# Kernel optimization log

Measured on AMD Instinct MI355X. Metric: run time of the kernel, lower is better.

## Reference

```python
import jax, jax.numpy as jnp
import numpy as np

B, BEV = 2, 128
Q = BEV * BEV          # 16384 BEV queries
C, H, L, P = 256, 8, 1, 4
D = C // H             # 32 per-head dim


def setup_inputs() -> dict:
    key = jax.random.key(0)
    ks = jax.random.split(key, 14)
    s = 0.02
    return {
        "query": jax.random.normal(ks[0], (B, Q, C), jnp.float32),
        "value": jax.random.normal(ks[1], (B, Q, C), jnp.float32),
        "identity": jax.random.normal(ks[2], (B, Q, C), jnp.float32),
        "query_pos": jax.random.normal(ks[3], (B, Q, C), jnp.float32),
        "reference_points": jax.random.uniform(ks[4], (B, Q, L, 2), jnp.float32),
        "spatial_shapes": jnp.array([[BEV, BEV]], jnp.int32),
        "level_start_index": jnp.array([0], jnp.int32),
        "Wv": jax.random.normal(ks[5], (C, C), jnp.float32) * s,
        "bv": jnp.zeros((C,), jnp.float32),
        "Woff": jax.random.normal(ks[6], (C, H * L * P * 2), jnp.float32) * s,
        "boff": jax.random.normal(ks[7], (H * L * P * 2,), jnp.float32) * s,
        "Ww": jax.random.normal(ks[8], (C, H * L * P), jnp.float32) * s,
        "bw": jnp.zeros((H * L * P,), jnp.float32),
        "Wo": jax.random.normal(ks[9], (C, C), jnp.float32) * s,
        "bo": jnp.zeros((C,), jnp.float32),
    }


def _deform_attn(q, v, reference_points, shapes_np, Wv, bv, Woff, boff, Ww, bw, Wo, bo):
    b, nq, _ = q.shape
    v = v @ Wv + bv                                             # value_proj
    off = (q @ Woff + boff).reshape(b, nq, H, L, P, 2)          # sampling offsets
    attn = jax.nn.softmax((q @ Ww + bw).reshape(b, nq, H, L * P), axis=-1)
    attn = attn.reshape(b, nq, H, L, P)
    # offset normalizer is (W, H) per level
    norm = jnp.asarray(shapes_np[:, ::-1], jnp.float32)         # [L, 2]
    loc = reference_points[:, :, None, :, None, :] + off / norm[None, None, None, :, None, :]

    out = jnp.zeros((b, H, nq, D), jnp.float32)
    start = 0
    for l in range(L):
        Hl, Wl = int(shapes_np[l, 0]), int(shapes_np[l, 1])
        N = Hl * Wl
        vl = v[:, start:start + N].reshape(b, N, H, D).transpose(0, 2, 1, 3)  # [b,H,N,D]
        start += N
        ll = loc[:, :, :, l]                                    # [b,nq,H,P,2] in [0,1]
        # grid_sample(align_corners=False): pixel coord = loc*size - 0.5
        x = ll[..., 0] * Wl - 0.5
        y = ll[..., 1] * Hl - 0.5
        x0 = jnp.floor(x); y0 = jnp.floor(y)
        dx = x - x0; dy = y - y0
        x0i = x0.astype(jnp.int32); y0i = y0.astype(jnp.int32)

        def gather(ix, iy):
            valid = (ix >= 0) & (ix < Wl) & (iy >= 0) & (iy < Hl)  # zero padding
            idx = jnp.clip(iy, 0, Hl - 1) * Wl + jnp.clip(ix, 0, Wl - 1)
            idx = idx.transpose(0, 2, 1, 3).reshape(b, H, nq * P)
            g = jnp.take_along_axis(vl, idx[..., None], axis=2)   # [b,H,nq*P,D]
            return g * valid.transpose(0, 2, 1, 3).reshape(b, H, nq * P, 1)

        def cw(w):  # corner weight -> [b,H,nq*P,1]
            return w.transpose(0, 2, 1, 3).reshape(b, H, nq * P, 1)

        samp = (gather(x0i, y0i) * cw((1 - dx) * (1 - dy))
                + gather(x0i + 1, y0i) * cw(dx * (1 - dy))
                + gather(x0i, y0i + 1) * cw((1 - dx) * dy)
                + gather(x0i + 1, y0i + 1) * cw(dx * dy))
        samp = samp.reshape(b, H, nq, P, D)
        aw = attn[:, :, :, l].transpose(0, 2, 1, 3)             # [b,H,nq,P]
        out = out + jnp.einsum('bhqpd,bhqp->bhqd', samp, aw)

    out = out.transpose(0, 2, 1, 3).reshape(b, nq, C)
    return out @ Wo + bo                                        # output_proj


def reference(query, value, identity, query_pos, reference_points, spatial_shapes,
              level_start_index, Wv, bv, Woff, boff, Ww, bw, Wo, bo):
    shapes_np = np.asarray(spatial_shapes)                      # static level shapes
    q = query + query_pos
    out = _deform_attn(q, value, reference_points, shapes_np,
                       Wv, bv, Woff, boff, Ww, bw, Wo, bo)
    return out + identity
```

## Files before the change

### kernel.cpp

```cpp
#include <hip/hip_runtime.h>
#include <hip/hip_bf16.h>
#include <stdint.h>

#define Q_TOT 32768
#define CC 256
#define GRID_W 128
#define GRID_H 128

typedef __attribute__((ext_vector_type(8))) short short8;
typedef __attribute__((ext_vector_type(4))) float floatx4;

__device__ __forceinline__ ushort f2bf(float f) {
    union { float f; uint32_t u; } v; v.f = f;
    uint32_t r = (v.u + 0x7fffu + ((v.u >> 16) & 1u)) >> 16;
    return (ushort)r;
}
__device__ __forceinline__ void bf2x2(uint32_t u, float& lo, float& hi) {
    union { uint32_t u; float f; } a, b;
    a.u = u << 16; b.u = u & 0xffff0000u;
    lo = a.f; hi = b.f;
}
__device__ __forceinline__ void async_load16(const void* g, void* l) {
    __builtin_amdgcn_global_load_lds(
        reinterpret_cast<const __attribute__((address_space(1))) uint32_t*>(
            reinterpret_cast<uintptr_t>(g)),
        reinterpret_cast<__attribute__((address_space(3))) uint32_t*>(
            reinterpret_cast<uintptr_t>(l)),
        16, 0, 0);
}

__global__ __launch_bounds__(256)
void prep_weights(const float* __restrict__ Wv, const float* __restrict__ Wo,
                  const float* __restrict__ Woff, const float* __restrict__ Ww,
                  const float* __restrict__ boff, const float* __restrict__ bw,
                  ushort* __restrict__ WvT, ushort* __restrict__ WoT,
                  ushort* __restrict__ WowT, float* __restrict__ bias_ow)
{
    int idx = blockIdx.x * blockDim.x + threadIdx.x;
    if (idx < 65536) {
        int n = idx >> 8, k = idx & 255;
        WvT[idx] = f2bf(Wv[k * 256 + n]);
    } else if (idx < 131072) {
        int t = idx - 65536; int n = t >> 8, k = t & 255;
        WoT[t] = f2bf(Wo[k * 256 + n]);
    } else if (idx < 155648) {
        int t = idx - 131072; int n = t >> 8, k = t & 255;
        float v = (n < 64) ? Woff[k * 64 + n] : Ww[k * 32 + (n - 64)];
        WowT[t] = f2bf(v);
    } else if (idx < 155744) {
        int t = idx - 155648;
        bias_ow[t] = (t < 64) ? boff[t] : bw[t - 64];
    }
}

template <int BM, int BN, int WAVE_M, int WAVE_N, bool OUT_BF16, int CONV>
__global__ __launch_bounds__(256)
void gemm_bf16(const void* __restrict__ Av, const float* __restrict__ A2,
               const ushort* __restrict__ Bt,
               const float* __restrict__ bias, const float* __restrict__ res,
               void* __restrict__ Cout, int M, int N, int K)
{
    constexpr int TM = BM / WAVE_M / 16;
    constexpr int TN = BN / WAVE_N / 16;
    __shared__ __align__(16) ushort As[2][BM * 32];
    __shared__ __align__(16) ushort Bs[2][BN * 32];

    const int tid = threadIdx.x;
    const int lane = tid & 63;
    const int wave = tid >> 6;
    const int wm = wave / WAVE_N;
    const int wn = wave % WAVE_N;
    const int quad = lane >> 4;
    const int m16 = lane & 15;
    const int lrow = lane >> 2;
    const int lkk = (lane & 3) * 8;

    const int nwg = gridDim.x * gridDim.y;
    const int hw = blockIdx.y * gridDim.x + blockIdx.x;
    const int t = (hw & 7) * (nwg >> 3) + (hw >> 3);
    const int bx = t % gridDim.x;
    const int by = t / gridDim.x;

    const int row0 = by * BM;
    const int col0 = bx * BN;

    floatx4 acc[TM][TN] = {};

    auto stage = [&](int buf, int k0) {
        #pragma unroll
        for (int i = wave; i < BM / 16; i += 4) {
            const int r = row0 + i * 16 + lrow;
            if constexpr (CONV == 0) {
                const ushort* src = (const ushort*)Av + (size_t)r * K + (k0 + lkk);
                async_load16(src, &As[buf][i * 16 * 32]);
            } else {
                const float* src = (const float*)Av + (size_t)r * K + (k0 + lkk);
                float4 a0 = ((const float4*)src)[0];
                float4 a1 = ((const float4*)src)[1];
                if constexpr (CONV == 2) {
                    const float* s2 = A2 + (size_t)r * K + (k0 + lkk);
                    float4 b0 = ((const float4*)s2)[0];
                    float4 b1 = ((const float4*)s2)[1];
                    a0.x += b0.x; a0.y += b0.y; a0.z += b0.z; a0.w += b0.w;
                    a1.x += b1.x; a1.y += b1.y; a1.z += b1.z; a1.w += b1.w;
                }
                uint4 o;
                o.x = ((uint32_t)f2bf(a0.y) << 16) | f2bf(a0.x);
                o.y = ((uint32_t)f2bf(a0.w) << 16) | f2bf(a0.z);
                o.z = ((uint32_t)f2bf(a1.y) << 16) | f2bf(a1.x);
                o.w = ((uint32_t)f2bf(a1.w) << 16) | f2bf(a1.z);
                *(uint4*)&As[buf][i * 16 * 32 + lrow * 32 + lkk] = o;
            }
        }
        #pragma unroll
        for (int i = wave; i < BN / 16; i += 4) {
            const ushort* src = Bt + (size_t)(col0 + i * 16 + lrow) * K + (k0 + lkk);
            async_load16(src, &Bs[buf][i * 16 * 32]);
        }
    };

    stage(0, 0);
    __syncthreads();

    int cur = 0;
    for (int k0 = 0; k0 < K; k0 += 32) {
        if (k0 + 32 < K) stage(cur ^ 1, k0 + 32);

        short8 af[TM], bfr[TN];
        #pragma unroll
        for (int i = 0; i < TM; ++i)
            af[i] = *(const short8*)&As[cur][(wm * TM * 16 + i * 16 + m16) * 32 + quad * 8];
        #pragma unroll
        for (int j = 0; j < TN; ++j)
            bfr[j] = *(const short8*)&Bs[cur][(wn * TN * 16 + j * 16 + m16) * 32 + quad * 8];
        #pragma unroll
        for (int i = 0; i < TM; ++i)
            #pragma unroll
            for (int j = 0; j < TN; ++j)
                acc[i][j] = __builtin_amdgcn_mfma_f32_16x16x32_bf16(
                    af[i], bfr[j], acc[i][j], 0, 0, 0);

        __syncthreads();
        cur ^= 1;
    }

    #pragma unroll
    for (int i = 0; i < TM; ++i) {
        #pragma unroll
        for (int j = 0; j < TN; ++j) {
            const int gcol = col0 + wn * TN * 16 + j * 16 + m16;
            const float bb = bias[gcol];
            #pragma unroll
            for (int r = 0; r < 4; ++r) {
                const int grow = row0 + wm * TM * 16 + i * 16 + quad * 4 + r;
                float v = acc[i][j][r] + bb;
                if (res) v += res[(size_t)grow * N + gcol];
                if constexpr (OUT_BF16)
                    ((ushort*)Cout)[(size_t)grow * N + gcol] = f2bf(v);
                else
                    ((float*)Cout)[(size_t)grow * N + gcol] = v;
            }
        }
    }
}

#define QB 8
__global__ __launch_bounds__(256)
void sample_kernel(const ushort* __restrict__ v2,
                   const ushort* __restrict__ ow,
                   const float* __restrict__ ref,
                   ushort* __restrict__ out)
{
    const int tid = threadIdx.x;
    const int ql = tid >> 5;
    const int h  = (tid >> 2) & 7;
    const int dg = tid & 3;
    const int q = blockIdx.x * QB + ql;
    const int b = q >> 14;

    const ushort* op = ow + (size_t)q * 96 + h * 8;
    const uint4 oraw = *(const uint4*)op;
    float offs[8];
    bf2x2(oraw.x, offs[0], offs[1]);
    bf2x2(oraw.y, offs[2], offs[3]);
    bf2x2(oraw.z, offs[4], offs[5]);
    bf2x2(oraw.w, offs[6], offs[7]);

    const uint2 wraw = *(const uint2*)(ow + (size_t)q * 96 + 64 + h * 4);
    float w0, w1, w2, w3;
    bf2x2(wraw.x, w0, w1);
    bf2x2(wraw.y, w2, w3);
    float m = fmaxf(fmaxf(w0, w1), fmaxf(w2, w3));
    float e0 = __expf(w0 - m), e1 = __expf(w1 - m), e2 = __expf(w2 - m), e3 = __expf(w3 - m);
    float inv = 1.f / (e0 + e1 + e2 + e3);
    float aw[4] = {e0 * inv, e1 * inv, e2 * inv, e3 * inv};

    const float rx = ref[(size_t)q * 2 + 0];
    const float ry = ref[(size_t)q * 2 + 1];
    const ushort* vb = v2 + (size_t)b * 16384 * 256 + h * 32 + dg * 8;

    float acc[8] = {};
    #pragma unroll
    for (int p = 0; p < 4; ++p) {
        float x = rx * (float)GRID_W + offs[p * 2 + 0] - 0.5f;
        float y = ry * (float)GRID_H + offs[p * 2 + 1] - 0.5f;
        float x0f = floorf(x), y0f = floorf(y);
        float dx = x - x0f, dy = y - y0f;
        int x0 = (int)x0f, y0 = (int)y0f;
        int x1 = x0 + 1, y1 = y0 + 1;
        float vx0 = (x0 >= 0 && x0 < GRID_W) ? 1.f : 0.f;
        float vx1 = (x1 >= 0 && x1 < GRID_W) ? 1.f : 0.f;
        float vy0 = (y0 >= 0 && y0 < GRID_H) ? 1.f : 0.f;
        float vy1 = (y1 >= 0 && y1 < GRID_H) ? 1.f : 0.f;
        int xc0 = min(max(x0, 0), GRID_W - 1), xc1 = min(max(x1, 0), GRID_W - 1);
        int yc0 = min(max(y0, 0), GRID_H - 1), yc1 = min(max(y1, 0), GRID_H - 1);
        float cw00 = aw[p] * (1.f - dx) * (1.f - dy) * vx0 * vy0;
        float cw10 = aw[p] * dx * (1.f - dy) * vx1 * vy0;
        float cw01 = aw[p] * (1.f - dx) * dy * vx0 * vy1;
        float cw11 = aw[p] * dx * dy * vx1 * vy1;
        const int base0 = yc0 * GRID_W, base1 = yc1 * GRID_W;
        const uint4 r00 = *(const uint4*)(vb + (size_t)(base0 + xc0) * 256);
        const uint4 r10 = *(const uint4*)(vb + (size_t)(base0 + xc1) * 256);
        const uint4 r01 = *(const uint4*)(vb + (size_t)(base1 + xc0) * 256);
        const uint4 r11 = *(const uint4*)(vb + (size_t)(base1 + xc1) * 256);
        float lo, hi;
        bf2x2(r00.x, lo, hi); acc[0] += cw00 * lo; acc[1] += cw00 * hi;
        bf2x2(r00.y, lo, hi); acc[2] += cw00 * lo; acc[3] += cw00 * hi;
        bf2x2(r00.z, lo, hi); acc[4] += cw00 * lo; acc[5] += cw00 * hi;
        bf2x2(r00.w, lo, hi); acc[6] += cw00 * lo; acc[7] += cw00 * hi;
        bf2x2(r10.x, lo, hi); acc[0] += cw10 * lo; acc[1] += cw10 * hi;
        bf2x2(r10.y, lo, hi); acc[2] += cw10 * lo; acc[3] += cw10 * hi;
        bf2x2(r10.z, lo, hi); acc[4] += cw10 * lo; acc[5] += cw10 * hi;
        bf2x2(r10.w, lo, hi); acc[6] += cw10 * lo; acc[7] += cw10 * hi;
        bf2x2(r01.x, lo, hi); acc[0] += cw01 * lo; acc[1] += cw01 * hi;
        bf2x2(r01.y, lo, hi); acc[2] += cw01 * lo; acc[3] += cw01 * hi;
        bf2x2(r01.z, lo, hi); acc[4] += cw01 * lo; acc[5] += cw01 * hi;
        bf2x2(r01.w, lo, hi); acc[6] += cw01 * lo; acc[7] += cw01 * hi;
        bf2x2(r11.x, lo, hi); acc[0] += cw11 * lo; acc[1] += cw11 * hi;
        bf2x2(r11.y, lo, hi); acc[2] += cw11 * lo; acc[3] += cw11 * hi;
        bf2x2(r11.z, lo, hi); acc[4] += cw11 * lo; acc[5] += cw11 * hi;
        bf2x2(r11.w, lo, hi); acc[6] += cw11 * lo; acc[7] += cw11 * hi;
    }

    uint4 o;
    o.x = ((uint32_t)f2bf(acc[1]) << 16) | f2bf(acc[0]);
    o.y = ((uint32_t)f2bf(acc[3]) << 16) | f2bf(acc[2]);
    o.z = ((uint32_t)f2bf(acc[5]) << 16) | f2bf(acc[4]);
    o.w = ((uint32_t)f2bf(acc[7]) << 16) | f2bf(acc[6]);
    *(uint4*)(out + (size_t)q * 256 + h * 32 + dg * 8) = o;
}

extern "C" void kernel_launch(void* const* d_in, const int* in_sizes, int n_in,
                              void* d_out, int out_size, void* d_ws, size_t ws_size,
                              hipStream_t stream) {
    const float* query     = (const float*)d_in[0];
    const float* value     = (const float*)d_in[1];
    const float* identity  = (const float*)d_in[2];
    const float* query_pos = (const float*)d_in[3];
    const float* refpts    = (const float*)d_in[4];
    const float* Wv   = (const float*)d_in[7];
    const float* bv   = (const float*)d_in[8];
    const float* Woff = (const float*)d_in[9];
    const float* boff = (const float*)d_in[10];
    const float* Ww   = (const float*)d_in[11];
    const float* bw   = (const float*)d_in[12];
    const float* Wo   = (const float*)d_in[13];
    const float* bo   = (const float*)d_in[14];
    float* out = (float*)d_out;

    char* ws = (char*)d_ws;
    ushort* v2_bf    = (ushort*)(ws);
    ushort* ow_bf    = (ushort*)(ws + 16777216);
    ushort* samp_bf  = (ushort*)(ws + 23068672);
    ushort* WvT      = (ushort*)(ws + 39845888);
    ushort* WoT      = (ushort*)(ws + 39976960);
    ushort* WowT     = (ushort*)(ws + 40108032);
    float*  bias_ow  = (float*)(ws + 40157184);

    prep_weights<<<609, 256, 0, stream>>>(Wv, Wo, Woff, Ww, boff, bw,
                                          WvT, WoT, WowT, bias_ow);
    gemm_bf16<128, 64, 2, 2, true, 1><<<dim3(4, 256), 256, 0, stream>>>(
        value, nullptr, WvT, bv, nullptr, v2_bf, Q_TOT, 256, 256);
    gemm_bf16<32, 96, 2, 2, true, 2><<<dim3(1, 1024), 256, 0, stream>>>(
        query, query_pos, WowT, bias_ow, nullptr, ow_bf, Q_TOT, 96, 256);
    sample_kernel<<<dim3(Q_TOT / QB), 256, 0, stream>>>(v2_bf, ow_bf, refpts, samp_bf);
    gemm_bf16<128, 64, 2, 2, false, 0><<<dim3(4, 256), 256, 0, stream>>>(
        samp_bf, nullptr, WoT, bo, identity, out, Q_TOT, 256, 256);
}
```

Baseline: 253.9 us.

## Fuse offset/weight projection, bilinear sampling and output projection into one kernel

After: 230.5 us. -9.2%, faster.

```diff
diff --git a/kernel.cpp b/kernel.cpp
--- a/kernel.cpp
+++ b/kernel.cpp
@@ -32,9 +32,8 @@
 __global__ __launch_bounds__(256)
 void prep_weights(const float* __restrict__ Wv, const float* __restrict__ Wo,
                   const float* __restrict__ Woff, const float* __restrict__ Ww,
-                  const float* __restrict__ boff, const float* __restrict__ bw,
                   ushort* __restrict__ WvT, ushort* __restrict__ WoT,
-                  ushort* __restrict__ WowT, float* __restrict__ bias_ow)
+                  ushort* __restrict__ WowT)
 {
     int idx = blockIdx.x * blockDim.x + threadIdx.x;
     if (idx < 65536) {
@@ -47,9 +46,6 @@
         int t = idx - 131072; int n = t >> 8, k = t & 255;
         float v = (n < 64) ? Woff[k * 64 + n] : Ww[k * 32 + (n - 64)];
         WowT[t] = f2bf(v);
-    } else if (idx < 155744) {
-        int t = idx - 155648;
-        bias_ow[t] = (t < 64) ? boff[t] : bw[t - 64];
     }
 }
 
@@ -164,90 +160,208 @@
     }
 }
 
-#define QB 8
+#define FBM 64
 __global__ __launch_bounds__(256)
-void sample_kernel(const ushort* __restrict__ v2,
-                   const ushort* __restrict__ ow,
-                   const float* __restrict__ ref,
-                   ushort* __restrict__ out)
+void fused_attn(const float* __restrict__ query, const float* __restrict__ qpos,
+                const ushort* __restrict__ WowT,
+                const float* __restrict__ boff, const float* __restrict__ bw,
+                const ushort* __restrict__ v2,
+                const float* __restrict__ ref,
+                const ushort* __restrict__ WoT,
+                const float* __restrict__ bo, const float* __restrict__ identity,
+                float* __restrict__ out)
 {
+    __shared__ __align__(16) char smem[71680];
+    ushort* As   = (ushort*)smem;
+    ushort* Bsow = (ushort*)(smem + 4096);
+    float*  owl  = (float*)(smem + 10240);
+    ushort* samp = (ushort*)(smem + 36864);
+    ushort* Bwo  = (ushort*)smem;
+
     const int tid = threadIdx.x;
-    const int ql = tid >> 5;
-    const int h  = (tid >> 2) & 7;
-    const int dg = tid & 3;
-    const int q = blockIdx.x * QB + ql;
-    const int b = q >> 14;
-
-    const ushort* op = ow + (size_t)q * 96 + h * 8;
-    const uint4 oraw = *(const uint4*)op;
-    float offs[8];
-    bf2x2(oraw.x, offs[0], offs[1]);
-    bf2x2(oraw.y, offs[2], offs[3]);
-    bf2x2(oraw.z, offs[4], offs[5]);
-    bf2x2(oraw.w, offs[6], offs[7]);
-
-    const uint2 wraw = *(const uint2*)(ow + (size_t)q * 96 + 64 + h * 4);
-    float w0, w1, w2, w3;
-    bf2x2(wraw.x, w0, w1);
-    bf2x2(wraw.y, w2, w3);
-    float m = fmaxf(fmaxf(w0, w1), fmaxf(w2, w3));
-    float e0 = __expf(w0 - m), e1 = __expf(w1 - m), e2 = __expf(w2 - m), e3 = __expf(w3 - m);
-    float inv = 1.f / (e0 + e1 + e2 + e3);
-    float aw[4] = {e0 * inv, e1 * inv, e2 * inv, e3 * inv};
-
-    const float rx = ref[(size_t)q * 2 + 0];
-    const float ry = ref[(size_t)q * 2 + 1];
-    const ushort* vb = v2 + (size_t)b * 16384 * 256 + h * 32 + dg * 8;
-
-    float acc[8] = {};
+    const int lane = tid & 63;
+    const int wave = tid >> 6;
+    const int quad = lane >> 4;
+    const int m16 = lane & 15;
+    const int lrow = lane >> 2;
+    const int lkk = (lane & 3) * 8;
+    const int wm = wave >> 1;
+    const int wn = wave & 1;
+
+    const int q0 = blockIdx.x * FBM;
+
+    floatx4 aow[2][3] = {};
+    for (int k0 = 0; k0 < 256; k0 += 32) {
+        {
+            const int r = wave * 16 + lrow;
+            const float* s1 = query + (size_t)(q0 + r) * 256 + (k0 + lkk);
+            const float* s2 = qpos  + (size_t)(q0 + r) * 256 + (k0 + lkk);
+            float4 a0 = ((const float4*)s1)[0];
+            float4 a1 = ((const float4*)s1)[1];
+            float4 b0 = ((const float4*)s2)[0];
+            float4 b1 = ((const float4*)s2)[1];
+            a0.x += b0.x; a0.y += b0.y; a0.z += b0.z; a0.w += b0.w;
+            a1.x += b1.x; a1.y += b1.y; a1.z += b1.z; a1.w += b1.w;
+            uint4 o;
+            o.x = ((uint32_t)f2bf(a0.y) << 16) | f2bf(a0.x);
+            o.y = ((uint32_t)f2bf(a0.w) << 16) | f2bf(a0.z);
+            o.z = ((uint32_t)f2bf(a1.y) << 16) | f2bf(a1.x);
+            o.w = ((uint32_t)f2bf(a1.w) << 16) | f2bf(a1.z);
+            *(uint4*)&As[r * 32 + lkk] = o;
+        }
+        for (int i = wave; i < 6; i += 4) {
+            const ushort* src = WowT + (size_t)(i * 16 + lrow) * 256 + (k0 + lkk);
+            async_load16(src, &Bsow[i * 16 * 32]);
+        }
+        __syncthreads();
+
+        short8 af[2], bfw[3];
+        #pragma unroll
+        for (int i = 0; i < 2; ++i)
+            af[i] = *(const short8*)&As[(wm * 32 + i * 16 + m16) * 32 + quad * 8];
+        #pragma unroll
+        for (int j = 0; j < 3; ++j)
+            bfw[j] = *(const short8*)&Bsow[(wn * 48 + j * 16 + m16) * 32 + quad * 8];
+        #pragma unroll
+        for (int i = 0; i < 2; ++i)
+            #pragma unroll
+            for (int j = 0; j < 3; ++j)
+                aow[i][j] = __builtin_amdgcn_mfma_f32_16x16x32_bf16(
+                    af[i], bfw[j], aow[i][j], 0, 0, 0);
+        __syncthreads();
+    }
     #pragma unroll
-    for (int p = 0; p < 4; ++p) {
-        float x = rx * (float)GRID_W + offs[p * 2 + 0] - 0.5f;
-        float y = ry * (float)GRID_H + offs[p * 2 + 1] - 0.5f;
-        float x0f = floorf(x), y0f = floorf(y);
-        float dx = x - x0f, dy = y - y0f;
-        int x0 = (int)x0f, y0 = (int)y0f;
-        int x1 = x0 + 1, y1 = y0 + 1;
-        float vx0 = (x0 >= 0 && x0 < GRID_W) ? 1.f : 0.f;
-        float vx1 = (x1 >= 0 && x1 < GRID_W) ? 1.f : 0.f;
-        float vy0 = (y0 >= 0 && y0 < GRID_H) ? 1.f : 0.f;
-        float vy1 = (y1 >= 0 && y1 < GRID_H) ? 1.f : 0.f;
-        int xc0 = min(max(x0, 0), GRID_W - 1), xc1 = min(max(x1, 0), GRID_W - 1);
-        int yc0 = min(max(y0, 0), GRID_H - 1), yc1 = min(max(y1, 0), GRID_H - 1);
-        float cw00 = aw[p] * (1.f - dx) * (1.f - dy) * vx0 * vy0;
-        float cw10 = aw[p] * dx * (1.f - dy) * vx1 * vy0;
-        float cw01 = aw[p] * (1.f - dx) * dy * vx0 * vy1;
-        float cw11 = aw[p] * dx * dy * vx1 * vy1;
-        const int base0 = yc0 * GRID_W, base1 = yc1 * GRID_W;
-        const uint4 r00 = *(const uint4*)(vb + (size_t)(base0 + xc0) * 256);
-        const uint4 r10 = *(const uint4*)(vb + (size_t)(base0 + xc1) * 256);
-        const uint4 r01 = *(const uint4*)(vb + (size_t)(base1 + xc0) * 256);
-        const uint4 r11 = *(const uint4*)(vb + (size_t)(base1 + xc1) * 256);
-        float lo, hi;
-        bf2x2(r00.x, lo, hi); acc[0] += cw00 * lo; acc[1] += cw00 * hi;
-        bf2x2(r00.y, lo, hi); acc[2] += cw00 * lo; acc[3] += cw00 * hi;
-        bf2x2(r00.z, lo, hi); acc[4] += cw00 * lo; acc[5] += cw00 * hi;
-        bf2x2(r00.w, lo, hi); acc[6] += cw00 * lo; acc[7] += cw00 * hi;
-        bf2x2(r10.x, lo, hi); acc[0] += cw10 * lo; acc[1] += cw10 * hi;
-        bf2x2(r10.y, lo, hi); acc[2] += cw10 * lo; acc[3] += cw10 * hi;
-        bf2x2(r10.z, lo, hi); acc[4] += cw10 * lo; acc[5] += cw10 * hi;
-        bf2x2(r10.w, lo, hi); acc[6] += cw10 * lo; acc[7] += cw10 * hi;
-        bf2x2(r01.x, lo, hi); acc[0] += cw01 * lo; acc[1] += cw01 * hi;
-        bf2x2(r01.y, lo, hi); acc[2] += cw01 * lo; acc[3] += cw01 * hi;
-        bf2x2(r01.z, lo, hi); acc[4] += cw01 * lo; acc[5] += cw01 * hi;
-        bf2x2(r01.w, lo, hi); acc[6] += cw01 * lo; acc[7] += cw01 * hi;
-        bf2x2(r11.x, lo, hi); acc[0] += cw11 * lo; acc[1] += cw11 * hi;
-        bf2x2(r11.y, lo, hi); acc[2] += cw11 * lo; acc[3] += cw11 * hi;
-        bf2x2(r11.z, lo, hi); acc[4] += cw11 * lo; acc[5] += cw11 * hi;
-        bf2x2(r11.w, lo, hi); acc[6] += cw11 * lo; acc[7] += cw11 * hi;
-    }
-
-    uint4 o;
-    o.x = ((uint32_t)f2bf(acc[1]) << 16) | f2bf(acc[0]);
-    o.y = ((uint32_t)f2bf(acc[3]) << 16) | f2bf(acc[2]);
-    o.z = ((uint32_t)f2bf(acc[5]) << 16) | f2bf(acc[4]);
-    o.w = ((uint32_t)f2bf(acc[7]) << 16) | f2bf(acc[6]);
-    *(uint4*)(out + (size_t)q * 256 + h * 32 + dg * 8) = o;
+    for (int i = 0; i < 2; ++i)
+        #pragma unroll
+        for (int j = 0; j < 3; ++j) {
+            const int col = wn * 48 + j * 16 + m16;
+            const float bb = (col < 64) ? boff[col] : bw[col - 64];
+            #pragma unroll
+            for (int r = 0; r < 4; ++r)
+                owl[(wm * 32 + i * 16 + quad * 4 + r) * 104 + col] = aow[i][j][r] + bb;
+        }
+    __syncthreads();
+
+    {
+        const int ql = tid >> 2;
+        const int dg = tid & 3;
+        const int qg = q0 + ql;
+        const int bb2 = qg >> 14;
+        const float rx = ref[(size_t)qg * 2 + 0] * (float)GRID_W;
+        const float ry = ref[(size_t)qg * 2 + 1] * (float)GRID_H;
+        const ushort* vbase = v2 + (size_t)bb2 * 16384 * 256 + dg * 8;
+        const float* owr = &owl[ql * 104];
+
+        #pragma unroll 1
+        for (int h = 0; h < 8; ++h) {
+            const float w0 = owr[64 + h * 4 + 0], w1 = owr[64 + h * 4 + 1];
+            const float w2 = owr[64 + h * 4 + 2], w3 = owr[64 + h * 4 + 3];
+            const float mx = fmaxf(fmaxf(w0, w1), fmaxf(w2, w3));
+            const float e0 = __expf(w0 - mx), e1 = __expf(w1 - mx);
+            const float e2 = __expf(w2 - mx), e3 = __expf(w3 - mx);
+            const float inv = 1.f / (e0 + e1 + e2 + e3);
+            const float aw[4] = {e0 * inv, e1 * inv, e2 * inv, e3 * inv};
+
+            const ushort* vh = vbase + h * 32;
+            float acc8[8] = {};
+            #pragma unroll
+            for (int p = 0; p < 4; ++p) {
+                const float x = rx + owr[h * 8 + p * 2 + 0] - 0.5f;
+                const float y = ry + owr[h * 8 + p * 2 + 1] - 0.5f;
+                const float x0f = floorf(x), y0f = floorf(y);
+                const float dx = x - x0f, dy = y - y0f;
+                const int x0 = (int)x0f, y0 = (int)y0f;
+                const int x1 = x0 + 1, y1 = y0 + 1;
+                const float vx0 = (x0 >= 0 && x0 < GRID_W) ? 1.f : 0.f;
+                const float vx1 = (x1 >= 0 && x1 < GRID_W) ? 1.f : 0.f;
+                const float vy0 = (y0 >= 0 && y0 < GRID_H) ? 1.f : 0.f;
+                const float vy1 = (y1 >= 0 && y1 < GRID_H) ? 1.f : 0.f;
+                const int xc0 = min(max(x0, 0), GRID_W - 1);
+                const int xc1 = min(max(x1, 0), GRID_W - 1);
+                const int yc0 = min(max(y0, 0), GRID_H - 1);
+                const int yc1 = min(max(y1, 0), GRID_H - 1);
+                const float cw00 = aw[p] * (1.f - dx) * (1.f - dy) * vx0 * vy0;
+                const float cw10 = aw[p] * dx * (1.f - dy) * vx1 * vy0;
+                const float cw01 = aw[p] * (1.f - dx) * dy * vx0 * vy1;
+                const float cw11 = aw[p] * dx * dy * vx1 * vy1;
+                const int base0 = yc0 * GRID_W, base1 = yc1 * GRID_W;
+                const uint4 r00 = *(const uint4*)(vh + (size_t)(base0 + xc0) * 256);
+                const uint4 r10 = *(const uint4*)(vh + (size_t)(base0 + xc1) * 256);
+                const uint4 r01 = *(const uint4*)(vh + (size_t)(base1 + xc0) * 256);
+                const uint4 r11 = *(const uint4*)(vh + (size_t)(base1 + xc1) * 256);
+                float lo, hi;
+                bf2x2(r00.x, lo, hi); acc8[0] += cw00 * lo; acc8[1] += cw00 * hi;
+                bf2x2(r00.y, lo, hi); acc8[2] += cw00 * lo; acc8[3] += cw00 * hi;
+                bf2x2(r00.z, lo, hi); acc8[4] += cw00 * lo; acc8[5] += cw00 * hi;
+                bf2x2(r00.w, lo, hi); acc8[6] += cw00 * lo; acc8[7] += cw00 * hi;
+                bf2x2(r10.x, lo, hi); acc8[0] += cw10 * lo; acc8[1] += cw10 * hi;
+                bf2x2(r10.y, lo, hi); acc8[2] += cw10 * lo; acc8[3] += cw10 * hi;
+                bf2x2(r10.z, lo, hi); acc8[4] += cw10 * lo; acc8[5] += cw10 * hi;
+                bf2x2(r10.w, lo, hi); acc8[6] += cw10 * lo; acc8[7] += cw10 * hi;
+                bf2x2(r01.x, lo, hi); acc8[0] += cw01 * lo; acc8[1] += cw01 * hi;
+                bf2x2(r01.y, lo, hi); acc8[2] += cw01 * lo; acc8[3] += cw01 * hi;
+                bf2x2(r01.z, lo, hi); acc8[4] += cw01 * lo; acc8[5] += cw01 * hi;
+                bf2x2(r01.w, lo, hi); acc8[6] += cw01 * lo; acc8[7] += cw01 * hi;
+                bf2x2(r11.x, lo, hi); acc8[0] += cw11 * lo; acc8[1] += cw11 * hi;
+                bf2x2(r11.y, lo, hi); acc8[2] += cw11 * lo; acc8[3] += cw11 * hi;
+                bf2x2(r11.z, lo, hi); acc8[4] += cw11 * lo; acc8[5] += cw11 * hi;
+                bf2x2(r11.w, lo, hi); acc8[6] += cw11 * lo; acc8[7] += cw11 * hi;
+            }
+            uint4 o;
+            o.x = ((uint32_t)f2bf(acc8[1]) << 16) | f2bf(acc8[0]);
+            o.y = ((uint32_t)f2bf(acc8[3]) << 16) | f2bf(acc8[2]);
+            o.z = ((uint32_t)f2bf(acc8[5]) << 16) | f2bf(acc8[4]);
+            o.w = ((uint32_t)f2bf(acc8[7]) << 16) | f2bf(acc8[6]);
+            *(uint4*)&samp[ql * 272 + h * 32 + dg * 8] = o;
+        }
+    }
+    __syncthreads();
+
+    auto stageW = [&](int buf, int ks) {
+        for (int i = wave; i < 16; i += 4) {
+            const ushort* src = WoT + (size_t)(i * 16 + lrow) * 256 + ks * 32 + lkk;
+            async_load16(src, &Bwo[buf * 8192 + i * 16 * 32]);
+        }
+    };
+    stageW(0, 0);
+    __syncthreads();
+
+    floatx4 acc[2][8] = {};
+    int cur = 0;
+    for (int ks = 0; ks < 8; ++ks) {
+        if (ks + 1 < 8) stageW(cur ^ 1, ks + 1);
+
+        short8 af[2], bfr[8];
+        #pragma unroll
+        for (int i = 0; i < 2; ++i)
+            af[i] = *(const short8*)&samp[(wm * 32 + i * 16 + m16) * 272 + ks * 32 + quad * 8];
+        #pragma unroll
+        for (int j = 0; j < 8; ++j)
+            bfr[j] = *(const short8*)&Bwo[cur * 8192 + (wn * 128 + j * 16 + m16) * 32 + quad * 8];
+        #pragma unroll
+        for (int i = 0; i < 2; ++i)
+            #pragma unroll
+            for (int j = 0; j < 8; ++j)
+                acc[i][j] = __builtin_amdgcn_mfma_f32_16x16x32_bf16(
+                    af[i], bfr[j], acc[i][j], 0, 0, 0);
+
+        __syncthreads();
+        cur ^= 1;
+    }
+
+    #pragma unroll
+    for (int i = 0; i < 2; ++i)
+        #pragma unroll
+        for (int j = 0; j < 8; ++j) {
+            const int gcol = wn * 128 + j * 16 + m16;
+            const float bb = bo[gcol];
+            #pragma unroll
+            for (int r = 0; r < 4; ++r) {
+                const int grow = q0 + wm * 32 + i * 16 + quad * 4 + r;
+                out[(size_t)grow * 256 + gcol] =
+                    acc[i][j][r] + bb + identity[(size_t)grow * 256 + gcol];
+            }
+        }
 }
 
 extern "C" void kernel_launch(void* const* d_in, const int* in_sizes, int n_in,
@@ -269,21 +383,14 @@
     float* out = (float*)d_out;
 
     char* ws = (char*)d_ws;
-    ushort* v2_bf    = (ushort*)(ws);
-    ushort* ow_bf    = (ushort*)(ws + 16777216);
-    ushort* samp_bf  = (ushort*)(ws + 23068672);
-    ushort* WvT      = (ushort*)(ws + 39845888);
-    ushort* WoT      = (ushort*)(ws + 39976960);
-    ushort* WowT     = (ushort*)(ws + 40108032);
-    float*  bias_ow  = (float*)(ws + 40157184);
-
-    prep_weights<<<609, 256, 0, stream>>>(Wv, Wo, Woff, Ww, boff, bw,
-                                          WvT, WoT, WowT, bias_ow);
+    ushort* v2_bf = (ushort*)(ws);
+    ushort* WvT   = (ushort*)(ws + 16777216);
+    ushort* WoT   = (ushort*)(ws + 16908288);
+    ushort* WowT  = (ushort*)(ws + 17039360);
+
+    prep_weights<<<608, 256, 0, stream>>>(Wv, Wo, Woff, Ww, WvT, WoT, WowT);
     gemm_bf16<128, 64, 2, 2, true, 1><<<dim3(4, 256), 256, 0, stream>>>(
         value, nullptr, WvT, bv, nullptr, v2_bf, Q_TOT, 256, 256);
-    gemm_bf16<32, 96, 2, 2, true, 2><<<dim3(1, 1024), 256, 0, stream>>>(
-        query, query_pos, WowT, bias_ow, nullptr, ow_bf, Q_TOT, 96, 256);
-    sample_kernel<<<dim3(Q_TOT / QB), 256, 0, stream>>>(v2_bf, ow_bf, refpts, samp_bf);
-    gemm_bf16<128, 64, 2, 2, false, 0><<<dim3(4, 256), 256, 0, stream>>>(
-        samp_bf, nullptr, WoT, bo, identity, out, Q_TOT, 256, 256);
-}
+    fused_attn<<<dim3(Q_TOT / FBM), 256, 0, stream>>>(
+        query, query_pos, WowT, boff, bw, v2_bf, refpts, WoT, bo, identity, out);
+}
```
